# Performance work log

Measured on AMD Instinct MI355X. Metric: run time of the kernel, lower is better.

The kernel has to match this reference:

```python
import jax, jax.numpy as jnp
import numpy as np

N, NS, B = 4096, 256, 2
X, Y, Z = 128, 128, 16
R = 4                      # compress_ratio per spatial axis
C, NC, H = 128, 20, 8      # feat dim, num classes, heads
DH = C // H
EPS = 1e-5


def setup_inputs() -> dict:
    rng = np.random.default_rng(0)
    gx_n, gy_n, gz_n = X // R, Y // R, Z // R
    # pick NS//B unique super-voxel cells per batch element
    cells = np.stack([rng.choice(gx_n * gy_n * gz_n, NS // B, replace=False) for _ in range(B)])
    gx = cells // (gy_n * gz_n)
    rem = cells % (gy_n * gz_n)
    gy, gz = rem // gz_n, rem % gz_n
    bidx = np.repeat(np.arange(B), NS // B)
    sv = np.stack([bidx, gx.ravel(), gy.ravel(), gz.ravel()], axis=1)  # [NS,4]
    per = N // NS  # 16 voxels per super-voxel, distinct offsets in the 4x4x4 cell
    offs = np.argsort(rng.random((NS, R * R * R)), axis=1)[:, :per]
    dx, dy, dz = offs // (R * R), (offs // R) % R, offs % R
    vox = np.stack([
        np.repeat(sv[:, 0], per),
        (sv[:, 1, None] * R + dx).ravel(),
        (sv[:, 2, None] * R + dy).ravel(),
        (sv[:, 3, None] * R + dz).ravel()], axis=1).astype(np.int32)

    ks = jax.random.split(jax.random.key(0), 12)
    p = lambda k, shape, s=0.02: jax.random.normal(k, shape, jnp.float32) * s
    return dict(
        indices=jnp.asarray(vox),
        features=jax.random.normal(ks[0], (N, C), jnp.float32),
        cw1=p(ks[1], (C, C)), cb1=jnp.zeros(C), cg1=jnp.ones(C), cbe1=jnp.zeros(C),
        cw2=p(ks[2], (C, C)), cb2=jnp.zeros(C),
        pw1=p(ks[3], (3, 64)), pb1=jnp.zeros(64), pg1=jnp.ones(64), pbe1=jnp.zeros(64),
        pw2=p(ks[4], (64, 1)), pb2=jnp.zeros(1),
        wq=p(ks[5], (C, C)), bq=jnp.zeros(C),
        wk=p(ks[6], (C, C)), bk=jnp.zeros(C),
        wv=p(ks[7], (C, C)), bv=jnp.zeros(C),
        wo=p(ks[8], (C, C)), bo=jnp.zeros(C),
        ln_g=jnp.ones(C), ln_b=jnp.zeros(C),
        seg_w=p(ks[9], (3, 3, 3, C, NC)), seg_b=jnp.zeros(NC),
    )


def _bn(x, g, b):  # BatchNorm1d, training-mode batch statistics
    mu = x.mean(0)
    var = x.var(0)
    return (x - mu) * jax.lax.rsqrt(var + EPS) * g + b


def reference(indices, features, cw1, cb1, cg1, cbe1, cw2, cb2,
              pw1, pb1, pg1, pbe1, pw2, pb2,
              wq, bq, wk, bk, wv, bv, wo, bo, ln_g, ln_b, seg_w, seg_b):
    ratio = jnp.array([1, R, R, R], dtype=indices.dtype)
    comp = indices // ratio                                  # [N,4] super-voxel coord
    unq, inv = jnp.unique(comp, axis=0, size=NS, return_inverse=True)
    # scatter-add softmax(features) over super-voxels
    cf = jax.ops.segment_sum(jax.nn.softmax(features, axis=1), inv, num_segments=NS)
    h = jax.nn.relu(_bn(cf @ cw1 + cb1, cg1, cbe1)) @ cw2 + cb2      # [NS,C]
    # pairwise relative-position bias: tiny MLP over [N*NS,3]
    pos = (indices[:, None, 1:] - unq[None, :, 1:]).astype(jnp.float32).reshape(N * NS, 3)
    pbias = (jax.nn.relu(_bn(pos @ pw1 + pb1, pg1, pbe1)) @ pw2 + pb2).reshape(N, NS)
    # multi-head cross attention: voxels query super-voxels, bias added to scores
    q = (features @ wq + bq).reshape(N, H, DH)
    k = (h @ wk + bk).reshape(NS, H, DH)
    v = (h @ wv + bv).reshape(NS, H, DH)
    scores = jnp.einsum('nhd,shd->hns', q, k) / np.float32(np.sqrt(DH)) + pbias[None]
    attn = jax.nn.softmax(scores, axis=-1)                   # [H,N,NS]
    ctx = jnp.einsum('hns,shd->nhd', attn, v).reshape(N, C) @ wo + bo
    y = features + ctx                                       # residual + LayerNorm sublayer
    mu = y.mean(-1, keepdims=True)
    var = y.var(-1, keepdims=True)
    y = (y - mu) * jax.lax.rsqrt(var + EPS) * ln_g + ln_b
    # SubMConv3d(128->20, k=3, pad=1): dense scatter -> conv -> gather at active sites
    grid = jnp.zeros((B, X, Y, Z, C), jnp.float32).at[
        indices[:, 0], indices[:, 1], indices[:, 2], indices[:, 3]].set(y)
    out = jax.lax.conv_general_dilated(
        grid, seg_w, (1, 1, 1), 'SAME',
        dimension_numbers=('NDHWC', 'DHWIO', 'NDHWC')) + seg_b
    return out[indices[:, 0], indices[:, 1], indices[:, 2], indices[:, 3]]  # [N,NC]
```

## Files before the change

kernel.cpp:

```cpp
#include <hip/hip_runtime.h>

typedef unsigned short ushort_t;

#define NVOX 4096
#define NSV  256
#define XD   128
#define YD   128
#define ZD   16
#define CD   128
#define NCD  20
#define HD   8
#define DHD  16
#define MAPN 524288
#define EPSF 1e-5f

#define OF_FEAT 0
#define OF_CW1  524288
#define OF_CB1  540672
#define OF_CG1  540800
#define OF_CBE1 540928
#define OF_CW2  541056
#define OF_CB2  557440
#define OF_PW1  557568
#define OF_PB1  557760
#define OF_PG1  557824
#define OF_PBE1 557888
#define OF_PW2  557952
#define OF_PB2  558016
#define OF_WQ   558080
#define OF_BQ   574464
#define OF_WK   574592
#define OF_BK   590976
#define OF_WV   591104
#define OF_BV   607488
#define OF_WO   607616
#define OF_BO   624000
#define OF_LNG  624128
#define OF_LNB  624256
#define OF_SEGW 624384
#define OF_SEGB 693504
#define ARENA_N 693568
#define TOTCVT2 100053

__device__ __forceinline__ float bf2f(const ushort_t* p){
  return __uint_as_float(((unsigned)(*p)) << 16);
}
__device__ __forceinline__ ushort_t f2bf(float f){
  unsigned u = __float_as_uint(f);
  u += 0x7fffu + ((u >> 16) & 1u);
  return (ushort_t)(u >> 16);
}
__device__ __forceinline__ float unlo(unsigned u){ return __uint_as_float(u << 16); }
__device__ __forceinline__ float unhi(unsigned u){ return __uint_as_float(u & 0xffff0000u); }

struct SrcPtrs { const void* p[25]; };

__device__ const int g_cnt2[24] = {16384,128,128,128,16384,128,192,64,64,64,64,1,
                                   16384,128,16384,128,16384,128,16384,128,128,128,0,20};
__device__ const int g_off2[24] = {OF_CW1,OF_CB1,OF_CG1,OF_CBE1,OF_CW2,OF_CB2,
                                   OF_PW1,OF_PB1,OF_PG1,OF_PBE1,OF_PW2,OF_PB2,
                                   OF_WQ,OF_BQ,OF_WK,OF_BK,OF_WV,OF_BV,OF_WO,OF_BO,
                                   OF_LNG,OF_LNB,OF_SEGW,OF_SEGB};

__device__ __forceinline__ float ldi(const void* p, int off, int fl){
  return fl ? bf2f((const ushort_t*)p + off) : ((const float*)p)[off];
}

struct SPREP {
  float frows[16][CD];
  float qpart[2][16][CD];
  float part[8][CD];
  float cfs[CD];
  float gpart[8][CD];
};
union __align__(16) UPREP { SPREP sv; int smom[18]; };

__global__ __launch_bounds__(512) void kprep(SrcPtrs sp, const int* idx, int* flag,
    float* arena, float* wt, int* map, float* afold_g, float* scfold_g,
    float* qb, float* t1T)
{
  __shared__ UPREP sm;
  __shared__ int sm_flag;
  int t = threadIdx.x, b = blockIdx.x;
  if (t < 64){
    const ushort_t* f16 = (const ushort_t*)sp.p[0];
    unsigned u = f16[2*t];
    int e = (u >> 7) & 0xFF;
    int sane = (u == 0 || (e >= 90 && e <= 150)) ? 1 : 0;
    unsigned long long bl = __ballot(sane);
    if (t == 0) sm_flag = (__popcll(bl) >= 48) ? 1 : 0;
  }
  __syncthreads();
  const int fl = sm_flag;

  if (b < 255){
    int gid = b*512 + t;
    const int GS = 255*512;
    if (gid == 0) *flag = fl;
    for (int k=gid; k<MAPN; k+=GS) map[k] = -1;
    for (int el=gid; el<TOTCVT2; el+=GS){
      int s=0, rem=el;
      while (rem >= g_cnt2[s]){ rem -= g_cnt2[s]; ++s; }
      arena[g_off2[s]+rem] = ldi(sp.p[s+1], rem, fl);
    }
    for (int k=gid; k<27*NCD*CD; k+=GS){
      int nb = k/(NCD*CD); int rem = k - nb*(NCD*CD); int o = rem/CD, i = rem - o*CD;
      wt[k] = ldi(sp.p[23], nb*(CD*NCD) + i*NCD + o, fl);
    }
  } else if (b < 511){
    int sv = b - 255;
    int rb = sv*16;
    if (fl){
      const uint2* fsrc = (const uint2*)((const ushort_t*)sp.p[0] + (size_t)rb*CD);
      uint2 u = fsrc[t];
      float* dst = &sm.sv.frows[t>>5][(t&31)*4];
      dst[0]=unlo(u.x); dst[1]=unhi(u.x); dst[2]=unlo(u.y); dst[3]=unhi(u.y);
    } else {
      const float4* fsrc = (const float4*)((const float*)sp.p[0] + (size_t)rb*CD);
      ((float4*)sm.sv.frows)[t] = fsrc[t];
    }
    __syncthreads();
    {
      int c8 = (t&15)*8, r = (t>>4)&15, kh = t>>8;
      int i0 = kh*64;
      float acc[8] = {0.f,0.f,0.f,0.f,0.f,0.f,0.f,0.f};
      if (fl){
        const ushort_t* wqp = (const ushort_t*)sp.p[13];
        #pragma unroll 4
        for (int i=i0; i<i0+64; ++i){
          uint4 w4 = *(const uint4*)(wqp + (size_t)i*CD + c8);
          float fr = sm.sv.frows[r][i];
          acc[0] += unlo(w4.x)*fr; acc[1] += unhi(w4.x)*fr;
          acc[2] += unlo(w4.y)*fr; acc[3] += unhi(w4.y)*fr;
          acc[4] += unlo(w4.z)*fr; acc[5] += unhi(w4.z)*fr;
          acc[6] += unlo(w4.w)*fr; acc[7] += unhi(w4.w)*fr;
        }
      } else {
        const float* wqp = (const float*)sp.p[13];
        #pragma unroll 4
        for (int i=i0; i<i0+64; ++i){
          float4 wa = *(const float4*)(wqp + (size_t)i*CD + c8);
          float4 wb = *(const float4*)(wqp + (size_t)i*CD + c8 + 4);
          float fr = sm.sv.frows[r][i];
          acc[0]+=wa.x*fr; acc[1]+=wa.y*fr; acc[2]+=wa.z*fr; acc[3]+=wa.w*fr;
          acc[4]+=wb.x*fr; acc[5]+=wb.y*fr; acc[6]+=wb.z*fr; acc[7]+=wb.w*fr;
        }
      }
      #pragma unroll
      for (int j=0;j<8;++j) sm.sv.qpart[kh][r][c8+j] = acc[j];
    }
    __syncthreads();
    for (int e = t; e < 16*CD; e += 512){
      int r = e>>7, c = e&127;
      qb[(size_t)(rb+r)*CD + c] = sm.sv.qpart[0][r][c] + sm.sv.qpart[1][r][c]
                                + ldi(sp.p[14], c, fl);
    }
    {
      int w = t>>6, l = t&63;
      float a0 = 0.f, a1 = 0.f;
      #pragma unroll
      for (int k=0;k<2;++k){
        int r = w*2 + k;
        float f0 = sm.sv.frows[r][l];
        float f1 = sm.sv.frows[r][l+64];
        float m = fmaxf(f0,f1);
        #pragma unroll
        for (int o=32;o;o>>=1) m = fmaxf(m, __shfl_xor(m,o,64));
        float e0 = __expf(f0-m), e1 = __expf(f1-m);
        float ssum = e0+e1;
        #pragma unroll
        for (int o=32;o;o>>=1) ssum += __shfl_xor(ssum,o,64);
        float inv = 1.f/ssum;
        a0 += e0*inv; a1 += e1*inv;
      }
      sm.sv.part[w][l] = a0; sm.sv.part[w][l+64] = a1;
    }
    __syncthreads();
    if (t < CD){
      float s = 0.f;
      #pragma unroll
      for (int w=0;w<8;++w) s += sm.sv.part[w][t];
      sm.sv.cfs[t] = s;
    }
    __syncthreads();
    {
      int c2 = (t&63)*2, kg = t>>6;
      int i0 = kg*16;
      float a0 = 0.f, a1 = 0.f;
      if (fl){
        const ushort_t* W = (const ushort_t*)sp.p[1];
        #pragma unroll 4
        for (int i=i0; i<i0+16; ++i){
          unsigned w = *(const unsigned*)(W + (size_t)i*CD + c2);
          float cfv = sm.sv.cfs[i];
          a0 += unlo(w)*cfv; a1 += unhi(w)*cfv;
        }
      } else {
        const float* W = (const float*)sp.p[1];
        #pragma unroll 4
        for (int i=i0; i<i0+16; ++i){
          float2 w = *(const float2*)(W + (size_t)i*CD + c2);
          float cfv = sm.sv.cfs[i];
          a0 += w.x*cfv; a1 += w.y*cfv;
        }
      }
      sm.sv.gpart[kg][c2] = a0; sm.sv.gpart[kg][c2+1] = a1;
    }
    __syncthreads();
    if (t < CD){
      float s = 0.f;
      #pragma unroll
      for (int kg=0;kg<8;++kg) s += sm.sv.gpart[kg][t];
      t1T[(size_t)t*NSV + sv] = s + ldi(sp.p[2], t, fl);
    }
  } else {
    if (t < 18) sm.smom[t] = 0;
    __syncthreads();
    {
      int sacc[9] = {0,0,0,0,0,0,0,0,0};
      for (int v = t; v < NVOX; v += 512){
        int4 q = ((const int4*)idx)[v];
        sacc[0]+=q.y; sacc[1]+=q.z; sacc[2]+=q.w;
        sacc[3]+=q.y*q.y; sacc[4]+=q.z*q.z; sacc[5]+=q.w*q.w;
        sacc[6]+=q.y*q.z; sacc[7]+=q.y*q.w; sacc[8]+=q.z*q.w;
      }
      int um[9] = {0,0,0,0,0,0,0,0,0};
      if (t < 256){
        int4 q = ((const int4*)idx)[t*16];
        int gx=q.y>>2, gy=q.z>>2, gz=q.w>>2;
        um[0]=gx; um[1]=gy; um[2]=gz;
        um[3]=gx*gx; um[4]=gy*gy; um[5]=gz*gz;
        um[6]=gx*gy; um[7]=gx*gz; um[8]=gy*gz;
      }
      int lane = t & 63;
      #pragma unroll
      for (int i=0;i<9;++i){
        int s = sacc[i];
        int u = um[i];
        #pragma unroll
        for (int o=32;o;o>>=1){
          s += __shfl_xor(s, o, 64);
          u += __shfl_xor(u, o, 64);
        }
        if (lane == 0){
          if (s) atomicAdd(&sm.smom[9+i], s);
          if (u) atomicAdd(&sm.smom[i], u);
        }
      }
    }
    __syncthreads();
    if (t < 64){
      int* smom = sm.smom;
      double U1[3]={(double)smom[0],(double)smom[1],(double)smom[2]};
      double S1[3]={(double)smom[9],(double)smom[10],(double)smom[11]};
      double Uxx[3][3], Sxx[3][3];
      Uxx[0][0]=smom[3]; Uxx[1][1]=smom[4]; Uxx[2][2]=smom[5];
      Uxx[0][1]=Uxx[1][0]=smom[6]; Uxx[0][2]=Uxx[2][0]=smom[7]; Uxx[1][2]=Uxx[2][1]=smom[8];
      Sxx[0][0]=smom[12]; Sxx[1][1]=smom[13]; Sxx[2][2]=smom[14];
      Sxx[0][1]=Sxx[1][0]=smom[15]; Sxx[0][2]=Sxx[2][0]=smom[16]; Sxx[1][2]=Sxx[2][1]=smom[17];
      double M1[3], M2[3][3];
      for (int a=0;a<3;++a) M1[a] = 256.0*S1[a] - 4096.0*U1[a];
      for (int a=0;a<3;++a)
        for (int b2=0;b2<3;++b2)
          M2[a][b2] = 256.0*Sxx[a][b2] - S1[a]*U1[b2] - S1[b2]*U1[a] + 4096.0*Uxx[a][b2];
      double wv_[3]={(double)ldi(sp.p[7],t,fl),(double)ldi(sp.p[7],64+t,fl),(double)ldi(sp.p[7],128+t,fl)};
      double bj=(double)ldi(sp.p[8],t,fl), gj=(double)ldi(sp.p[9],t,fl), bej=(double)ldi(sp.p[10],t,fl);
      double Mw=0.0, wMw=0.0;
      for (int a=0;a<3;++a){
        Mw += M1[a]*wv_[a];
        for (int b2=0;b2<3;++b2) wMw += wv_[a]*M2[a][b2]*wv_[b2];
      }
      const double NM = 1048576.0;
      double mean = Mw/NM + bj;
      double Ey2  = wMw/NM + 2.0*bj*Mw/NM + bj*bj;
      double var  = Ey2 - mean*mean;
      double scale = gj / sqrt(var + 1e-5);
      afold_g[t]      = (float)(wv_[0]*scale);
      afold_g[64+t]   = (float)(wv_[1]*scale);
      afold_g[128+t]  = (float)(wv_[2]*scale);
      scfold_g[t]     = (float)(bj*scale + bej - mean*scale);
    }
  }
}

__global__ __launch_bounds__(256) void k6pb(const float* t1T, const float* A,
    const int* idx, int* map, float* kb, float* vb,
    const float* afold_g, const float* scfold_g, float* pbias_b)
{
  __shared__ float saf[3][64];
  __shared__ float ssc[64];
  __shared__ float w2s[64];
  __shared__ __align__(16) float e4q[64][8];
  __shared__ float xs[8], ys[8], zs[8];
  __shared__ float row[CD];
  __shared__ float cpar[2][CD];
  __shared__ float hrow[CD];
  int t = threadIdx.x, b = blockIdx.x;
  if (b < 512){
    if (t < 64){
      saf[0][t] = afold_g[t]; saf[1][t] = afold_g[64+t]; saf[2][t] = afold_g[128+t];
      ssc[t] = scfold_g[t]; w2s[t] = A[OF_PW2+t];
    } else if (t < 72){
      int qi = t - 64;
      int4 q = ((const int4*)idx)[b*8 + qi];
      xs[qi] = (float)q.y; ys[qi] = (float)q.z; zs[qi] = (float)q.w;
    }
    __syncthreads();
    for (int e = t; e < 512; e += 256){
      int j = e & 63, qi = e >> 6;
      e4q[j][qi] = saf[0][j]*xs[qi] + saf[1][j]*ys[qi] + saf[2][j]*zs[qi];
    }
    __syncthreads();
    int4 q0 = ((const int4*)idx)[t*16];
    float ux = (float)(q0.y>>2), uy = (float)(q0.z>>2), uz = (float)(q0.w>>2);
    float pb2 = A[OF_PB2];
    float pbv[8];
    #pragma unroll
    for (int i=0;i<8;++i) pbv[i] = pb2;
    #pragma unroll 2
    for (int j=0;j<64;++j){
      float dj = ssc[j] - (saf[0][j]*ux + saf[1][j]*uy + saf[2][j]*uz);
      float wj = w2s[j];
      float4 e0 = *(const float4*)&e4q[j][0];
      float4 e1 = *(const float4*)&e4q[j][4];
      pbv[0] += fmaxf(e0.x+dj,0.f)*wj; pbv[1] += fmaxf(e0.y+dj,0.f)*wj;
      pbv[2] += fmaxf(e0.z+dj,0.f)*wj; pbv[3] += fmaxf(e0.w+dj,0.f)*wj;
      pbv[4] += fmaxf(e1.x+dj,0.f)*wj; pbv[5] += fmaxf(e1.y+dj,0.f)*wj;
      pbv[6] += fmaxf(e1.z+dj,0.f)*wj; pbv[7] += fmaxf(e1.w+dj,0.f)*wj;
    }
    float* dst = pbias_b + ((size_t)b*256 + t)*8;
    *(float4*)dst       = make_float4(pbv[0],pbv[1],pbv[2],pbv[3]);
    *(float4*)(dst + 4) = make_float4(pbv[4],pbv[5],pbv[6],pbv[7]);
    return;
  }
  int role = (b - 512) >> 8, s = (b - 512) & 255;
  if (role == 0 && t >= 128 && t < 144){
    int v = s*16 + (t-128);
    int4 q = ((const int4*)idx)[v];
    map[((q.x*XD + q.y)*YD + q.z)*ZD + q.w] = v;
  }
  if (t < CD){
    const float4* col = (const float4*)(t1T + (size_t)t*NSV);
    float sum=0.f, sq=0.f;
    #pragma unroll 8
    for (int i=0;i<NSV/4;++i){
      float4 v = col[i];
      sum += v.x+v.y+v.z+v.w;
      sq  += v.x*v.x+v.y*v.y+v.z*v.z+v.w*v.w;
    }
    float mean = sum*(1.f/256.f);
    float var  = sq*(1.f/256.f) - mean*mean;
    float scv = A[OF_CG1+t]*rsqrtf(var+EPSF);
    float shv = A[OF_CBE1+t] - mean*scv;
    row[t] = fmaxf(t1T[(size_t)t*NSV + s]*scv + shv, 0.f);
  }
  __syncthreads();
  int c = t&127, half = t>>7;
  {
    const float* W = A + OF_CW2;
    float acc = 0.f;
    #pragma unroll 8
    for (int i=half*64;i<half*64+64;++i) acc += row[i]*W[i*CD+c];
    cpar[half][c] = acc;
  }
  __syncthreads();
  if (t < CD) hrow[t] = cpar[0][t]+cpar[1][t]+A[OF_CB2+t];
  __syncthreads();
  {
    const float* W = role ? (A+OF_WV) : (A+OF_WK);
    float acc = 0.f;
    #pragma unroll 8
    for (int i=half*64;i<half*64+64;++i) acc += hrow[i]*W[i*CD+c];
    cpar[half][c] = acc;
  }
  __syncthreads();
  if (t < CD){
    float v = cpar[0][t]+cpar[1][t] + (role ? A[OF_BV+t] : A[OF_BK+t]);
    if (role) vb[(size_t)s*CD+t] = v; else kb[(size_t)s*CD+t] = v;
  }
}

#define CGRP(row,hh) (((hh) + ((row)>>1)) & 3)

__global__ __launch_bounds__(256, 6) void k9_attn(
    const float* A, const int* idx, const float* pbias_b,
    const float* kb, const float* vb, const float* qb,
    const void* featsrc, const int* flag, float* yb)
{
  __shared__ __align__(16) float q4s[4][CD];
  __shared__ __align__(16) float scf[NSV][16];
  __shared__ __align__(16) float ctxT[CD*4];
  __shared__ float cpart[4][4][64];
  __shared__ float rinv[32];
  int t = threadIdx.x;
  int n0 = blockIdx.x*4;
  const int fl = *flag;
  if (t < 128) ((float4*)q4s)[t] = ((const float4*)(qb + (size_t)n0*CD))[t];
  float4 pbq = *(const float4*)(pbias_b + ((size_t)(n0>>3)*256 + t)*8 + (n0&7));
  float pbv[4] = {pbq.x, pbq.y, pbq.z, pbq.w};
  __syncthreads();
  const float4* krow = (const float4*)(kb + (size_t)t*CD);
  #pragma unroll
  for (int p=0;p<2;++p){
    {
      #pragma unroll
      for (int hh=0; hh<4; ++hh){
        int h = p*4 + hh;
        float4 k0 = krow[h*4+0], k1 = krow[h*4+1], k2 = krow[h*4+2], k3 = krow[h*4+3];
        float pr[4];
        #pragma unroll
        for (int g=0; g<4; ++g){
          const float4* qg4 = (const float4*)&q4s[g][h*DHD];
          float4 qa = qg4[0], qbv = qg4[1], qc = qg4[2], qd = qg4[3];
          float dot = qa.x*k0.x + qa.y*k0.y + qa.z*k0.z + qa.w*k0.w
                    + qbv.x*k1.x + qbv.y*k1.y + qbv.z*k1.z + qbv.w*k1.w
                    + qc.x*k2.x + qc.y*k2.y + qc.z*k2.z + qc.w*k2.w
                    + qd.x*k3.x + qd.y*k3.y + qd.z*k3.z + qd.w*k3.w;
          pr[g] = __expf(dot*0.25f + pbv[g]);
        }
        *(float4*)&scf[t][CGRP(t,hh)*4] = make_float4(pr[0],pr[1],pr[2],pr[3]);
      }
    }
    __syncthreads();
    {
      int g = t>>6, lane = t&63;
      #pragma unroll
      for (int hh=0; hh<4; ++hh){
        float s0 = 0.f;
        #pragma unroll
        for (int k=0;k<4;++k){
          int r = lane + 64*k;
          s0 += scf[r][CGRP(r,hh)*4 + g];
        }
        #pragma unroll
        for (int o=32;o;o>>=1) s0 += __shfl_xor(s0,o,64);
        if (lane==0) rinv[g*8 + p*4 + hh] = 1.f/s0;
      }
    }
    {
      int q = t>>6, c = t&63;
      int hh = c>>4;
      const float* vcol = vb + p*64 + c;
      float a0=0.f, a1=0.f, a2=0.f, a3=0.f;
      #pragma unroll 4
      for (int s=q*64; s<q*64+64; ++s){
        float v = vcol[(size_t)s*CD];
        float4 pv = *(const float4*)&scf[s][CGRP(s,hh)*4];
        a0 += pv.x*v; a1 += pv.y*v; a2 += pv.z*v; a3 += pv.w*v;
      }
      cpart[q][0][c]=a0; cpart[q][1][c]=a1; cpart[q][2][c]=a2; cpart[q][3][c]=a3;
    }
    __syncthreads();
    {
      int gsel = t>>6, c = t&63;
      int ch = p*64 + c, h = ch>>4;
      ctxT[ch*4+gsel] = (cpart[0][gsel][c]+cpart[1][gsel][c]
                        +cpart[2][gsel][c]+cpart[3][gsel][c]) * rinv[gsel*8+h];
    }
  }
  __syncthreads();
  {
    int half=t>>7, c=t&127;
    const float* wo = A + OF_WO;
    float acc[4]={0.f,0.f,0.f,0.f};
    #pragma unroll 4
    for (int i=half*64;i<half*64+64;++i){
      float wv = wo[i*CD+c];
      float4 r = *(const float4*)&ctxT[i*4];
      acc[0]+=r.x*wv; acc[1]+=r.y*wv; acc[2]+=r.z*wv; acc[3]+=r.w*wv;
    }
    #pragma unroll
    for (int g=0;g<4;++g) cpart[(c>>6)*2 + half][g][c&63] = acc[g];
  }
  __syncthreads();
  if (t < CD){
    float bov = A[OF_BO+t];
    int chi = t>>6, cl = t&63;
    #pragma unroll
    for (int g=0;g<4;++g){
      float fv = fl ? bf2f((const ushort_t*)featsrc + (size_t)(n0+g)*CD + t)
                    : ((const float*)featsrc)[(size_t)(n0+g)*CD + t];
      ctxT[t*4+g] = cpart[chi*2+0][g][cl] + cpart[chi*2+1][g][cl] + bov + fv;
    }
  }
  __syncthreads();
  {
    int g = t>>6, lane = t&63;
    float x0 = ctxT[lane*4+g], x1 = ctxT[(lane+64)*4+g];
    float s1 = x0+x1, s2 = x0*x0+x1*x1;
    #pragma unroll
    for (int o=32;o;o>>=1){ s1 += __shfl_xor(s1,o,64); s2 += __shfl_xor(s2,o,64); }
    float mean = s1*(1.f/128.f);
    float var  = s2*(1.f/128.f) - mean*mean;
    float rs = rsqrtf(var + EPSF);
    yb[(size_t)(n0+g)*CD + lane]    = (x0-mean)*rs*A[OF_LNG+lane]    + A[OF_LNB+lane];
    yb[(size_t)(n0+g)*CD + lane+64] = (x1-mean)*rs*A[OF_LNG+lane+64] + A[OF_LNB+lane+64];
  }
}

__global__ __launch_bounds__(256) void k10_conv(const int* idx, const int* map,
    const float* yb, const float* A, const float* wt, const int* flag, void* outv)
{
  __shared__ int sco4[8][4];
  __shared__ int jn[8][27];
  __shared__ float partial[4][8][NCD];
  int t = threadIdx.x;
  int p0 = blockIdx.x*8;
  if (t < 32) ((int*)sco4)[t] = idx[4*p0 + t];
  __syncthreads();
  if (t < 216){
    int v = t/27, nb = t - v*27;
    int kd = nb/9, kh = (nb/3)%3, kw = nb%3;
    int bb = sco4[v][0];
    int nx = sco4[v][1]+kd-1, ny = sco4[v][2]+kh-1, nz = sco4[v][3]+kw-1;
    int j = -1;
    if ((unsigned)nx < XD && (unsigned)ny < YD && (unsigned)nz < ZD)
      j = map[((bb*XD+nx)*YD+ny)*ZD+nz];
    jn[v][nb] = j;
  }
  __syncthreads();
  int w = t>>6, l = t&63;
  int og = l & 3, cg = l >> 2;
  int c0 = cg*8;
  float acc[8][5];
  #pragma unroll
  for (int v=0;v<8;++v)
    #pragma unroll
    for (int oo=0;oo<5;++oo) acc[v][oo]=0.f;
  for (int nb = w; nb < 27; nb += 4){
    const float* wbase = wt + (size_t)nb*NCD*CD + c0;
    float4 wreg[10];
    #pragma unroll
    for (int oo=0;oo<5;++oo){
      wreg[oo*2]   = *(const float4*)(wbase + (size_t)(og*5+oo)*CD);
      wreg[oo*2+1] = *(const float4*)(wbase + (size_t)(og*5+oo)*CD + 4);
    }
    #pragma unroll
    for (int v=0; v<8; ++v){
      int j = jn[v][nb];
      if (j < 0) continue;
      const float4* y4 = (const float4*)(yb + (size_t)j*CD + c0);
      float4 ya = y4[0], ybb = y4[1];
      #pragma unroll
      for (int oo=0;oo<5;++oo){
        float4 wa = wreg[oo*2], wb = wreg[oo*2+1];
        acc[v][oo] += ya.x*wa.x + ya.y*wa.y + ya.z*wa.z + ya.w*wa.w
                    + ybb.x*wb.x + ybb.y*wb.y + ybb.z*wb.z + ybb.w*wb.w;
      }
    }
  }
  #pragma unroll
  for (int v=0;v<8;++v)
    #pragma unroll
    for (int oo=0;oo<5;++oo){
      float s = acc[v][oo];
      s += __shfl_xor(s, 4, 64);
      s += __shfl_xor(s, 8, 64);
      s += __shfl_xor(s, 16, 64);
      s += __shfl_xor(s, 32, 64);
      if (cg == 0) partial[w][v][og*5+oo] = s;
    }
  __syncthreads();
  if (t < 160){
    int v = t/20, o = t - v*20;
    float s = partial[0][v][o]+partial[1][v][o]+partial[2][v][o]+partial[3][v][o]
            + A[OF_SEGB+o];
    if (*flag) ((ushort_t*)outv)[(size_t)(p0+v)*NCD + o] = f2bf(s);
    else       ((float*)outv)[(size_t)(p0+v)*NCD + o]   = s;
  }
}

extern "C" void kernel_launch(void* const* d_in, const int* in_sizes, int n_in,
                              void* d_out, int out_size, void* d_ws, size_t ws_size,
                              hipStream_t stream) {
  const int* idx = (const int*)d_in[0];

  char* w = (char*)d_ws;
  size_t off = 0;
  #define ALLOC(name, type, count) \
    type* name = (type*)(w + off); off += (((size_t)(count)*sizeof(type)) + 255) & ~(size_t)255;
  ALLOC(flag,   int,   64)
  ALLOC(arena,  float, ARENA_N)
  ALLOC(wt,     float, 27*NCD*CD)
  ALLOC(map,    int,   MAPN)
  ALLOC(afold,  float, 192)
  ALLOC(scfold, float, 64)
  ALLOC(t1T,    float, CD*NSV)
  ALLOC(kb,     float, NSV*CD)
  ALLOC(vbuf,   float, NSV*CD)
  ALLOC(qb,     float, NVOX*CD)
  ALLOC(yb,     float, NVOX*CD)
  ALLOC(pbias_b,float, 512*256*8)
  #undef ALLOC
  (void)off; (void)ws_size; (void)n_in; (void)in_sizes; (void)out_size;

  SrcPtrs sp;
  for (int i=0;i<25;++i) sp.p[i] = d_in[i+1];

  kprep   <<<512, 512, 0, stream>>>(sp, idx, flag, arena, wt, map, afold, scfold, qb, t1T);
  k6pb    <<<1024, 256, 0, stream>>>(t1T, arena, idx, map, kb, vbuf, afold, scfold, pbias_b);
  k9_attn <<<NVOX/4, 256, 0, stream>>>(arena, idx, pbias_b, kb, vbuf, qb, d_in[1], flag, yb);
  k10_conv<<<NVOX/8, 256, 0, stream>>>(idx, map, yb, arena, wt, flag, d_out);
}
```

Measured before the change: 200.7 us.

## Process eight queries per attention block with 512 threads and XOR-swizzled scores

The attention kernel now handles 8 voxel queries per block with 512 threads instead of 4 queries with 256 threads. Each K row and V column loaded from global memory is therefore reused across twice as many queries, halving K/V and Wo traffic per query. The score tile layout changes from a rotating group index to an XOR swizzle to avoid LDS bank conflicts, and the reductions are split across more waves. The cost is higher LDS use and register pressure per block, which may lower occupancy.

After: 197.4 us. No clear change (-1.6%).

```diff
diff --git a/kernel.cpp b/kernel.cpp
--- a/kernel.cpp
+++ b/kernel.cpp
@@ -380,113 +380,126 @@
   }
 }
 
-#define CGRP(row,hh) (((hh) + ((row)>>1)) & 3)
-
-__global__ __launch_bounds__(256, 6) void k9_attn(
+__global__ __launch_bounds__(512, 4) void k9_attn(
     const float* A, const int* idx, const float* pbias_b,
     const float* kb, const float* vb, const float* qb,
     const void* featsrc, const int* flag, float* yb)
 {
-  __shared__ __align__(16) float q4s[4][CD];
-  __shared__ __align__(16) float scf[NSV][16];
-  __shared__ __align__(16) float ctxT[CD*4];
-  __shared__ float cpart[4][4][64];
-  __shared__ float rinv[32];
+  __shared__ __align__(16) float q8s[8][CD];
+  __shared__ __align__(16) float scf[NSV][32];
+  __shared__ __align__(16) float ctxT[CD*8];
+  __shared__ __align__(16) float cpart[4096];
+  __shared__ float rinv[64];
   int t = threadIdx.x;
-  int n0 = blockIdx.x*4;
+  int n0 = blockIdx.x*8;
   const int fl = *flag;
-  if (t < 128) ((float4*)q4s)[t] = ((const float4*)(qb + (size_t)n0*CD))[t];
-  float4 pbq = *(const float4*)(pbias_b + ((size_t)(n0>>3)*256 + t)*8 + (n0&7));
-  float pbv[4] = {pbq.x, pbq.y, pbq.z, pbq.w};
-  __syncthreads();
-  const float4* krow = (const float4*)(kb + (size_t)t*CD);
+  if (t < 256) ((float4*)q8s)[t] = ((const float4*)(qb + (size_t)n0*CD))[t];
+  int ts = t & 255, hp = t >> 8;
+  const float* pbp = pbias_b + ((size_t)blockIdx.x*256 + ts)*8;
+  float4 pbq0 = *(const float4*)pbp;
+  float4 pbq1 = *(const float4*)(pbp + 4);
+  float pb[8] = {pbq0.x,pbq0.y,pbq0.z,pbq0.w, pbq1.x,pbq1.y,pbq1.z,pbq1.w};
+  __syncthreads();
+  const float4* krow = (const float4*)(kb + (size_t)ts*CD);
   #pragma unroll
   for (int p=0;p<2;++p){
     {
       #pragma unroll
-      for (int hh=0; hh<4; ++hh){
+      for (int u=0; u<2; ++u){
+        int hh = hp*2 + u;
         int h = p*4 + hh;
         float4 k0 = krow[h*4+0], k1 = krow[h*4+1], k2 = krow[h*4+2], k3 = krow[h*4+3];
-        float pr[4];
+        float pr[8];
         #pragma unroll
-        for (int g=0; g<4; ++g){
-          const float4* qg4 = (const float4*)&q4s[g][h*DHD];
+        for (int g=0; g<8; ++g){
+          const float4* qg4 = (const float4*)&q8s[g][h*DHD];
           float4 qa = qg4[0], qbv = qg4[1], qc = qg4[2], qd = qg4[3];
           float dot = qa.x*k0.x + qa.y*k0.y + qa.z*k0.z + qa.w*k0.w
                     + qbv.x*k1.x + qbv.y*k1.y + qbv.z*k1.z + qbv.w*k1.w
                     + qc.x*k2.x + qc.y*k2.y + qc.z*k2.z + qc.w*k2.w
                     + qd.x*k3.x + qd.y*k3.y + qd.z*k3.z + qd.w*k3.w;
-          pr[g] = __expf(dot*0.25f + pbv[g]);
-        }
-        *(float4*)&scf[t][CGRP(t,hh)*4] = make_float4(pr[0],pr[1],pr[2],pr[3]);
-      }
-    }
-    __syncthreads();
-    {
-      int g = t>>6, lane = t&63;
+          pr[g] = __expf(dot*0.25f + pb[g]);
+        }
+        int c4a = (hh*2+0) ^ (ts&7);
+        int c4b = (hh*2+1) ^ (ts&7);
+        *(float4*)&scf[ts][c4a*4] = make_float4(pr[0],pr[1],pr[2],pr[3]);
+        *(float4*)&scf[ts][c4b*4] = make_float4(pr[4],pr[5],pr[6],pr[7]);
+      }
+    }
+    __syncthreads();
+    {
+      int w = t>>6, lane = t&63;
+      int qg = w>>2, j = w&3;
       #pragma unroll
       for (int hh=0; hh<4; ++hh){
+        int slot = hh*2 + qg;
         float s0 = 0.f;
         #pragma unroll
         for (int k=0;k<4;++k){
           int r = lane + 64*k;
-          s0 += scf[r][CGRP(r,hh)*4 + g];
+          s0 += scf[r][(slot ^ (r&7))*4 + j];
         }
         #pragma unroll
         for (int o=32;o;o>>=1) s0 += __shfl_xor(s0,o,64);
-        if (lane==0) rinv[g*8 + p*4 + hh] = 1.f/s0;
-      }
-    }
-    {
-      int q = t>>6, c = t&63;
-      int hh = c>>4;
+        if (lane==0) rinv[w*8 + p*4 + hh] = 1.f/s0;
+      }
+    }
+    {
+      int o = t>>6, c = t&63, hh = c>>4;
       const float* vcol = vb + p*64 + c;
-      float a0=0.f, a1=0.f, a2=0.f, a3=0.f;
+      float a[8] = {0.f,0.f,0.f,0.f,0.f,0.f,0.f,0.f};
+      int sA = hh*2+0, sB = hh*2+1;
       #pragma unroll 4
-      for (int s=q*64; s<q*64+64; ++s){
+      for (int s=o*32; s<o*32+32; ++s){
         float v = vcol[(size_t)s*CD];
-        float4 pv = *(const float4*)&scf[s][CGRP(s,hh)*4];
-        a0 += pv.x*v; a1 += pv.y*v; a2 += pv.z*v; a3 += pv.w*v;
-      }
-      cpart[q][0][c]=a0; cpart[q][1][c]=a1; cpart[q][2][c]=a2; cpart[q][3][c]=a3;
-    }
-    __syncthreads();
-    {
-      int gsel = t>>6, c = t&63;
-      int ch = p*64 + c, h = ch>>4;
-      ctxT[ch*4+gsel] = (cpart[0][gsel][c]+cpart[1][gsel][c]
-                        +cpart[2][gsel][c]+cpart[3][gsel][c]) * rinv[gsel*8+h];
+        float4 pvA = *(const float4*)&scf[s][(sA ^ (s&7))*4];
+        float4 pvB = *(const float4*)&scf[s][(sB ^ (s&7))*4];
+        a[0] += pvA.x*v; a[1] += pvA.y*v; a[2] += pvA.z*v; a[3] += pvA.w*v;
+        a[4] += pvB.x*v; a[5] += pvB.y*v; a[6] += pvB.z*v; a[7] += pvB.w*v;
+      }
+      #pragma unroll
+      for (int g=0;g<8;++g) cpart[o*512 + g*64 + c] = a[g];
+    }
+    __syncthreads();
+    {
+      int g = t>>6, c = t&63;
+      float s = 0.f;
+      #pragma unroll
+      for (int o=0;o<8;++o) s += cpart[o*512 + g*64 + c];
+      ctxT[(p*64+c)*8 + g] = s * rinv[g*8 + p*4 + (c>>4)];
     }
   }
   __syncthreads();
   {
-    int half=t>>7, c=t&127;
+    int kq = t>>7, c = t&127;
     const float* wo = A + OF_WO;
-    float acc[4]={0.f,0.f,0.f,0.f};
+    float acc[8] = {0.f,0.f,0.f,0.f,0.f,0.f,0.f,0.f};
     #pragma unroll 4
-    for (int i=half*64;i<half*64+64;++i){
+    for (int i=kq*32; i<kq*32+32; ++i){
       float wv = wo[i*CD+c];
-      float4 r = *(const float4*)&ctxT[i*4];
-      acc[0]+=r.x*wv; acc[1]+=r.y*wv; acc[2]+=r.z*wv; acc[3]+=r.w*wv;
-    }
-    #pragma unroll
-    for (int g=0;g<4;++g) cpart[(c>>6)*2 + half][g][c&63] = acc[g];
+      float4 r0 = *(const float4*)&ctxT[i*8];
+      float4 r1 = *(const float4*)&ctxT[i*8+4];
+      acc[0]+=r0.x*wv; acc[1]+=r0.y*wv; acc[2]+=r0.z*wv; acc[3]+=r0.w*wv;
+      acc[4]+=r1.x*wv; acc[5]+=r1.y*wv; acc[6]+=r1.z*wv; acc[7]+=r1.w*wv;
+    }
+    #pragma unroll
+    for (int g=0;g<8;++g) cpart[kq*1024 + g*128 + c] = acc[g];
   }
   __syncthreads();
   if (t < CD){
     float bov = A[OF_BO+t];
-    int chi = t>>6, cl = t&63;
-    #pragma unroll
-    for (int g=0;g<4;++g){
+    #pragma unroll
+    for (int g=0;g<8;++g){
       float fv = fl ? bf2f((const ushort_t*)featsrc + (size_t)(n0+g)*CD + t)
                     : ((const float*)featsrc)[(size_t)(n0+g)*CD + t];
-      ctxT[t*4+g] = cpart[chi*2+0][g][cl] + cpart[chi*2+1][g][cl] + bov + fv;
+      ctxT[t*8+g] = cpart[g*128+t] + cpart[1024+g*128+t] + cpart[2048+g*128+t]
+                  + cpart[3072+g*128+t] + bov + fv;
     }
   }
   __syncthreads();
   {
     int g = t>>6, lane = t&63;
-    float x0 = ctxT[lane*4+g], x1 = ctxT[(lane+64)*4+g];
+    float x0 = ctxT[lane*8+g], x1 = ctxT[(lane+64)*8+g];
     float s1 = x0+x1, s2 = x0*x0+x1*x1;
     #pragma unroll
     for (int o=32;o;o>>=1){ s1 += __shfl_xor(s1,o,64); s2 += __shfl_xor(s2,o,64); }
@@ -599,6 +612,6 @@
 
   kprep   <<<512, 512, 0, stream>>>(sp, idx, flag, arena, wt, map, afold, scfold, qb, t1T);
   k6pb    <<<1024, 256, 0, stream>>>(t1T, arena, idx, map, kb, vbuf, afold, scfold, pbias_b);
-  k9_attn <<<NVOX/4, 256, 0, stream>>>(arena, idx, pbias_b, kb, vbuf, qb, d_in[1], flag, yb);
+  k9_attn <<<NVOX/8, 512, 0, stream>>>(arena, idx, pbias_b, kb, vbuf, qb, d_in[1], flag, yb);
   k10_conv<<<NVOX/8, 256, 0, stream>>>(idx, map, yb, arena, wt, flag, d_out);
 }
```
